# Performance work log

Measured on AMD Instinct MI355X. Metric: run time of the kernel, lower is better.

Reference implementation:

```python
import jax, jax.numpy as jnp
import numpy as np

HIDDEN = 128
STATE = 64
ACTION = 16
D_IO = STATE + ACTION  # 80
BATCH = 4096
SEQ_LEN = 512


def setup_inputs() -> dict:
    key = jax.random.key(0)
    ks = jax.random.split(key, 7)
    s = 1.0 / np.sqrt(HIDDEN)
    return {
        "quantized_hn": jax.random.normal(ks[0], (BATCH, HIDDEN), jnp.float32),
        "W_ih": jax.random.uniform(ks[1], (4 * HIDDEN, D_IO), jnp.float32, -s, s),
        "W_hh": jax.random.uniform(ks[2], (4 * HIDDEN, HIDDEN), jnp.float32, -s, s),
        "b_ih": jax.random.uniform(ks[3], (4 * HIDDEN,), jnp.float32, -s, s),
        "b_hh": jax.random.uniform(ks[4], (4 * HIDDEN,), jnp.float32, -s, s),
        "W_fc": jax.random.uniform(ks[5], (D_IO, HIDDEN), jnp.float32, -s, s),
        "b_fc": jax.random.uniform(ks[6], (D_IO,), jnp.float32, -s, s),
        "seq_len": SEQ_LEN,
    }


def reference(quantized_hn, W_ih, W_hh, b_ih, b_hh, W_fc, b_fc, seq_len):
    B, H = quantized_hn.shape
    D = W_fc.shape[0]

    def step(carry, _):
        h, c, x = carry  # h,c: (B,H); x: (B,D)
        # PyTorch LSTM gate order: i, f, g, o
        gates = x @ W_ih.T + b_ih + h @ W_hh.T + b_hh  # (B, 4H)
        i, f, g, o = jnp.split(gates, 4, axis=-1)
        c_new = jax.nn.sigmoid(f) * c + jax.nn.sigmoid(i) * jnp.tanh(g)
        h_new = jax.nn.sigmoid(o) * jnp.tanh(c_new)
        y = h_new @ W_fc.T + b_fc  # (B, D) -> fed back as next input
        return (h_new, c_new, y), y

    h0 = quantized_hn
    c0 = jnp.zeros((B, H), quantized_hn.dtype)
    x0 = jnp.zeros((B, D), quantized_hn.dtype)
    _, ys = jax.lax.scan(step, (h0, c0, x0), None, length=seq_len)
    return jnp.transpose(ys, (1, 0, 2))  # (B, seq_len, D)
```

## Files before the change

### kernel.cpp

```cpp
#include <hip/hip_runtime.h>

typedef __bf16 bf16_t;
typedef __bf16 bf16x4 __attribute__((ext_vector_type(4)));
typedef __bf16 bf16x8 __attribute__((ext_vector_type(8)));
typedef float  f32x4  __attribute__((ext_vector_type(4)));

#define HID    128
#define DIO    80
#define G4     512
#define TSTEP  512
#define BB     16
#define NBATCH 4096
#define NBLK   (NBATCH / BB)
#define HSTR   136

#define NL2E  -1.4426950408889634f
#define P2L2E  2.8853900817779268f

__device__ bf16_t g_weff_frags[128 * 512];
__device__ bf16_t g_whh_frags[128 * 512];
__device__ bf16_t g_wfc_frags[20 * 512];
__device__ float  g_weff[G4 * HID];
__device__ float  g_beff[G4];
__device__ float  g_b1[G4];

__global__ void k_weff(const float* __restrict__ W_ih, const float* __restrict__ W_hh,
                       const float* __restrict__ b_ih, const float* __restrict__ b_hh,
                       const float* __restrict__ W_fc, const float* __restrict__ b_fc) {
  int gid = blockIdx.x * blockDim.x + threadIdx.x;
  int g = gid >> 7, k = gid & 127;
  float sc = ((g >> 7) == 2) ? P2L2E : NL2E;
  float acc = W_hh[g * HID + k];
#pragma unroll 8
  for (int d = 0; d < DIO; ++d)
    acc = fmaf(W_ih[g * DIO + d], W_fc[d * HID + k], acc);
  g_weff[g * HID + k] = acc * sc;
  if (k == 0) {
    float bb = b_ih[g] + b_hh[g];
    g_b1[g] = bb * sc;
    float be = bb;
    for (int d = 0; d < DIO; ++d) be = fmaf(W_ih[g * DIO + d], b_fc[d], be);
    g_beff[g] = be * sc;
  }
}

__global__ void k_frag(const float* __restrict__ W_hh, const float* __restrict__ W_fc) {
  int tile = blockIdx.x;
  int lane = threadIdx.x;
  int c = lane & 15, q = lane >> 4;
  if (tile < 128) {
    int gtile = tile >> 2, kt = tile & 3;
    int n = gtile * 16 + c;
#pragma unroll
    for (int j = 0; j < 8; ++j)
      g_weff_frags[tile * 512 + lane * 8 + j] = (bf16_t)g_weff[n * HID + kt * 32 + q * 8 + j];
  } else if (tile < 256) {
    int t2 = tile - 128;
    int gtile = t2 >> 2, kt = t2 & 3;
    int n = gtile * 16 + c;
    float sc = ((n >> 7) == 2) ? P2L2E : NL2E;
#pragma unroll
    for (int j = 0; j < 8; ++j)
      g_whh_frags[t2 * 512 + lane * 8 + j] = (bf16_t)(W_hh[n * HID + kt * 32 + q * 8 + j] * sc);
  } else {
    int t2 = tile - 256;
    int yt = t2 >> 2, kt = t2 & 3;
    int n = yt * 16 + c;
#pragma unroll
    for (int j = 0; j < 8; ++j)
      g_wfc_frags[t2 * 512 + lane * 8 + j] = (bf16_t)W_fc[n * HID + kt * 32 + q * 8 + j];
  }
}

__device__ __forceinline__ float fexp2(float x) { return __builtin_amdgcn_exp2f(x); }
__device__ __forceinline__ float frcp(float x)  { return __builtin_amdgcn_rcpf(x); }

#define MFMA16(A, B, C) __builtin_amdgcn_mfma_f32_16x16x32_bf16((A), (B), (C), 0, 0, 0)

#define TAILR(ACC, CST, HV, R)                                                         \
  do {                                                                                 \
    float Eg = fexp2(ACC[2][R]);                                             \
    float ag = 1.0f + Eg;                                                              \
    float Ei = fexp2(ACC[0][R]);                                             \
    float ai = 1.0f + Ei;                                                              \
    float Ef = fexp2(ACC[1][R]);                                             \
    float af = 1.0f + Ef;                                                              \
    float P1 = ai * ag;                                                                \
    float Rr = frcp(P1 * af);                                                          \
    float tg = __builtin_fmaf(Eg, P2L2E, -P2L2E);                       \
    float m2 = tg * af;                                                                \
    float u  = __builtin_fmaf(P1, CST[R], m2);                                         \
    float cn = u * Rr;                             \
    CST[R] = cn;                                                                       \
    float cc = fminf(cn, 80.0f);                              \
    float Ec = fexp2(cc);                                                    \
    float Eo = fexp2(ACC[3][R]);                                             \
    float R2 = frcp((1.0f + Eo) * (1.0f + Ec));                                        \
    HV[R] = (bf16_t)((Ec - 1.0f) * R2);                            \
  } while (0)

#define GKT_FIRST(K, SRC)                                                              \
  acc[0] = MFMA16(Wg[0][K], SRC, bias[0]); acc[1] = MFMA16(Wg[1][K], SRC, bias[1]);    \
  acc[2] = MFMA16(Wg[2][K], SRC, bias[2]); acc[3] = MFMA16(Wg[3][K], SRC, bias[3]);
#define GKT(K, SRC)                                                                    \
  acc[0] = MFMA16(Wg[0][K], SRC, acc[0]); acc[1] = MFMA16(Wg[1][K], SRC, acc[1]);      \
  acc[2] = MFMA16(Wg[2][K], SRC, acc[2]); acc[3] = MFMA16(Wg[3][K], SRC, acc[3]);

#define YEMIT(PRV)                                                                     \
  { f32x4 ya = MFMA16(Wy[0], PRV[0], ybias); ya = MFMA16(Wy[1], PRV[1], ya);           \
    ya = MFMA16(Wy[2], PRV[2], ya); ya = MFMA16(Wy[3], PRV[3], ya);                    \
    *(f32x4*)outp = ya; outp += DIO; }

__device__ __forceinline__ void poll_ge(volatile unsigned* vf, int base, unsigned need) {
  for (;;) {
    unsigned a = vf[base + 0], b = vf[base + 1], x = vf[base + 2], d = vf[base + 3];
    unsigned m0 = a < b ? a : b, m1 = x < d ? x : d;
    if ((m0 < m1 ? m0 : m1) >= need) break;
  }
  __builtin_amdgcn_sched_barrier(0);
}

__global__ __launch_bounds__(512, 2) void k_lstm(const float* __restrict__ h0,
                                                 const float* __restrict__ b_fc,
                                                 float* __restrict__ out) {
  __shared__ __align__(16) bf16_t hbuf[2][BB * HSTR];
  __shared__ unsigned hflags[8];
  volatile unsigned* vf = hflags;
  const int tid = threadIdx.x;
  const int lane = tid & 63;
  const int w = tid >> 6;
  const int c = lane & 15, q = lane >> 4;
  const int b0 = blockIdx.x * BB;
  const bool isHigh = (w >= 4);

  for (int i = tid; i < BB * HID; i += 512) {
    int r = i >> 7, k = i & 127;
    hbuf[0][r * HSTR + k] = (bf16_t)h0[(long)(b0 + r) * HID + k];
  }
  if (lane == 0) hflags[w] = 1;

  bf16x8 Wy[4];
  f32x4  ybias;
  if (w < 5) {
#pragma unroll
    for (int kt = 0; kt < 4; ++kt)
      Wy[kt] = *(const bf16x8*)&g_wfc_frags[(w * 4 + kt) * 512 + lane * 8];
#pragma unroll
    for (int r = 0; r < 4; ++r) ybias[r] = b_fc[w * 16 + q * 4 + r];
  }

  bf16x8 Wg[4][4];
  f32x4  bias[4];
  auto load_wg = [&](const bf16_t* frags, const float* bsrc) {
#pragma unroll
    for (int G = 0; G < 4; ++G) {
      int gtile = G * 8 + w;
#pragma unroll
      for (int r = 0; r < 4; ++r) bias[G][r] = bsrc[gtile * 16 + q * 4 + r];
#pragma unroll
      for (int kt = 0; kt < 4; ++kt)
        Wg[G][kt] = *(const bf16x8*)&frags[(gtile * 4 + kt) * 512 + lane * 8];
    }
  };

  f32x4 cst = (f32x4){0, 0, 0, 0};
  bf16x8 hfA[4], hfB[4];

  load_wg(g_whh_frags, g_b1);
  __syncthreads();

  float* outp = out + (long)(b0 + c) * TSTEP * DIO + w * 16 + q * 4;

#pragma unroll
  for (int kt = 0; kt < 4; ++kt)
    hfA[kt] = *(const bf16x8*)&hbuf[0][c * HSTR + kt * 32 + q * 8];
  {
    f32x4 acc[4];
    GKT_FIRST(0, hfA[0]); GKT(1, hfA[1]); GKT(2, hfA[2]); GKT(3, hfA[3]);
    bf16x4 hv;
    TAILR(acc, cst, hv, 0); TAILR(acc, cst, hv, 1);
    TAILR(acc, cst, hv, 2); TAILR(acc, cst, hv, 3);
    *(bf16x4*)&hbuf[1][c * HSTR + w * 16 + q * 4] = hv;
    asm volatile("s_waitcnt lgkmcnt(0)" ::: "memory");
    if (lane == 0) vf[w] = 2;
  }
  load_wg(g_weff_frags, g_beff);

#define ITER(RD, PR, T, EMIT)                                                          \
  do {                                                                                 \
    const int rb = ((T)-1) & 1, wb = (T)&1;                                            \
    f32x4 acc[4];                                                                      \
    if (!isHigh) {                                                                     \
      poll_ge(vf, 0, (unsigned)(T));                                                   \
      RD[0] = *(const bf16x8*)&hbuf[rb][c * HSTR + 0 * 32 + q * 8];                    \
      RD[1] = *(const bf16x8*)&hbuf[rb][c * HSTR + 1 * 32 + q * 8];                    \
      GKT_FIRST(0, RD[0]); GKT(1, RD[1]);                                              \
      poll_ge(vf, 4, (unsigned)(T));                                                   \
      RD[2] = *(const bf16x8*)&hbuf[rb][c * HSTR + 2 * 32 + q * 8];                    \
      RD[3] = *(const bf16x8*)&hbuf[rb][c * HSTR + 3 * 32 + q * 8];                    \
      if ((EMIT) && w < 5) YEMIT(PR);                                                  \
      GKT(2, RD[2]); GKT(3, RD[3]);                                                    \
    } else {                                                                           \
      poll_ge(vf, 4, (unsigned)(T));                                                   \
      RD[2] = *(const bf16x8*)&hbuf[rb][c * HSTR + 2 * 32 + q * 8];                    \
      RD[3] = *(const bf16x8*)&hbuf[rb][c * HSTR + 3 * 32 + q * 8];                    \
      GKT_FIRST(2, RD[2]); GKT(3, RD[3]);                                              \
      poll_ge(vf, 0, (unsigned)(T));                                                   \
      RD[0] = *(const bf16x8*)&hbuf[rb][c * HSTR + 0 * 32 + q * 8];                    \
      RD[1] = *(const bf16x8*)&hbuf[rb][c * HSTR + 1 * 32 + q * 8];                    \
      if ((EMIT) && w < 5) YEMIT(PR);                                                  \
      GKT(0, RD[0]); GKT(1, RD[1]);                                                    \
    }                                                                                  \
    bf16x4 hv;                                                                         \
    TAILR(acc, cst, hv, 0); TAILR(acc, cst, hv, 1);                                    \
    TAILR(acc, cst, hv, 2); TAILR(acc, cst, hv, 3);                                    \
    *(bf16x4*)&hbuf[wb][c * HSTR + w * 16 + q * 4] = hv;                     \
    asm volatile("s_waitcnt lgkmcnt(0)" ::: "memory");                                 \
    if (lane == 0) vf[w] = (unsigned)((T) + 1);                                        \
  } while (0)

  ITER(hfB, hfA, 2, false);
  for (int p = 0; p < 255; ++p) {
    ITER(hfA, hfB, 3 + 2 * p, true);
    ITER(hfB, hfA, 4 + 2 * p, true);
  }

  if (w < 5) {
    YEMIT(hfB);
    poll_ge(vf, 0, 513u);
    poll_ge(vf, 4, 513u);
#pragma unroll
    for (int kt = 0; kt < 4; ++kt)
      hfA[kt] = *(const bf16x8*)&hbuf[0][c * HSTR + kt * 32 + q * 8];
    f32x4 ya = MFMA16(Wy[0], hfA[0], ybias);
    ya = MFMA16(Wy[1], hfA[1], ya);
    ya = MFMA16(Wy[2], hfA[2], ya);
    ya = MFMA16(Wy[3], hfA[3], ya);
    *(f32x4*)outp = ya;
  }
#undef ITER
}

extern "C" void kernel_launch(void* const* d_in, const int* in_sizes, int n_in,
                              void* d_out, int out_size, void* d_ws, size_t ws_size,
                              hipStream_t stream) {
  const float* h0   = (const float*)d_in[0];
  const float* W_ih = (const float*)d_in[1];
  const float* W_hh = (const float*)d_in[2];
  const float* b_ih = (const float*)d_in[3];
  const float* b_hh = (const float*)d_in[4];
  const float* W_fc = (const float*)d_in[5];
  const float* b_fc = (const float*)d_in[6];
  float* out = (float*)d_out;

  k_weff<<<256, 256, 0, stream>>>(W_ih, W_hh, b_ih, b_hh, W_fc, b_fc);
  k_frag<<<276, 64, 0, stream>>>(W_hh, W_fc);
  k_lstm<<<NBLK, 512, 0, stream>>>(h0, b_fc, out);
}
```

Measured before the change: 1.026 ms.

## Use per-k-tile paired 16-bit flags with staggered waits, sleep polling and priority

Replaces the 8 per-wave 32-bit flags with 16-bit flags packed in pairs, so each 32-bit read covers the two waves producing one 32-column k-tile. Each wave waits for and consumes k-tiles one at a time, starting with a rotated tile order (w>>1), so it can begin its MFMAs as soon as any producer pair has finished instead of waiting for groups of four waves. Spin loops now call s_sleep, and waves 0-3 get raised priority. The rotation is meant to cut synchronization stalls in the recurrent dependency. The costs are four polls per step instead of two, sleep latency on wakeups, and code size from the four-way unrolled RUN variants.

```diff
diff --git a/kernel.cpp b/kernel.cpp
--- a/kernel.cpp
+++ b/kernel.cpp
@@ -111,33 +111,33 @@
     ya = MFMA16(Wy[2], PRV[2], ya); ya = MFMA16(Wy[3], PRV[3], ya);                    \
     *(f32x4*)outp = ya; outp += DIO; }
 
-__device__ __forceinline__ void poll_ge(volatile unsigned* vf, int base, unsigned need) {
-  for (;;) {
-    unsigned a = vf[base + 0], b = vf[base + 1], x = vf[base + 2], d = vf[base + 3];
-    unsigned m0 = a < b ? a : b, m1 = x < d ? x : d;
-    if ((m0 < m1 ? m0 : m1) >= need) break;
-  }
-  __builtin_amdgcn_sched_barrier(0);
-}
+#define POLLP(K, NEED)                                                                 \
+  do {                                                                                 \
+    unsigned _pw = vfp[K];                                                             \
+    if ((_pw & 0xFFFFu) < (unsigned)(NEED) || (_pw >> 16) < (unsigned)(NEED)) {        \
+      do { __builtin_amdgcn_s_sleep(1); _pw = vfp[K]; }                                \
+      while ((_pw & 0xFFFFu) < (unsigned)(NEED) || (_pw >> 16) < (unsigned)(NEED));    \
+    }                                                                                  \
+    __builtin_amdgcn_sched_barrier(0);                                                 \
+  } while (0)
 
 __global__ __launch_bounds__(512, 2) void k_lstm(const float* __restrict__ h0,
                                                  const float* __restrict__ b_fc,
                                                  float* __restrict__ out) {
   __shared__ __align__(16) bf16_t hbuf[2][BB * HSTR];
-  __shared__ unsigned hflags[8];
-  volatile unsigned* vf = hflags;
+  __shared__ __align__(4) unsigned short hfl[8];
+  volatile unsigned* vfp = (volatile unsigned*)hfl;
   const int tid = threadIdx.x;
   const int lane = tid & 63;
   const int w = tid >> 6;
   const int c = lane & 15, q = lane >> 4;
   const int b0 = blockIdx.x * BB;
-  const bool isHigh = (w >= 4);
 
   for (int i = tid; i < BB * HID; i += 512) {
     int r = i >> 7, k = i & 127;
     hbuf[0][r * HSTR + k] = (bf16_t)h0[(long)(b0 + r) * HID + k];
   }
-  if (lane == 0) hflags[w] = 1;
+  if (tid < 8) hfl[tid] = 1;
 
   bf16x8 Wy[4];
   f32x4  ybias;
@@ -168,6 +168,8 @@
 
   load_wg(g_whh_frags, g_b1);
   __syncthreads();
+
+  if (w < 4) __builtin_amdgcn_s_setprio(1);
 
   float* outp = out + (long)(b0 + c) * TSTEP * DIO + w * 16 + q * 4;
 
@@ -182,63 +184,60 @@
     TAILR(acc, cst, hv, 2); TAILR(acc, cst, hv, 3);
     *(bf16x4*)&hbuf[1][c * HSTR + w * 16 + q * 4] = hv;
     asm volatile("s_waitcnt lgkmcnt(0)" ::: "memory");
-    if (lane == 0) vf[w] = 2;
+    if (lane == 0) ((volatile unsigned short*)hfl)[w] = 2;
   }
   load_wg(g_weff_frags, g_beff);
 
-#define ITER(RD, PR, T, EMIT)                                                          \
+#define ITER_K(RD, PR, T, EMIT, KA, KB, KC, KD)                                        \
   do {                                                                                 \
     const int rb = ((T)-1) & 1, wb = (T)&1;                                            \
     f32x4 acc[4];                                                                      \
-    if (!isHigh) {                                                                     \
-      poll_ge(vf, 0, (unsigned)(T));                                                   \
-      RD[0] = *(const bf16x8*)&hbuf[rb][c * HSTR + 0 * 32 + q * 8];                    \
-      RD[1] = *(const bf16x8*)&hbuf[rb][c * HSTR + 1 * 32 + q * 8];                    \
-      GKT_FIRST(0, RD[0]); GKT(1, RD[1]);                                              \
-      poll_ge(vf, 4, (unsigned)(T));                                                   \
-      RD[2] = *(const bf16x8*)&hbuf[rb][c * HSTR + 2 * 32 + q * 8];                    \
-      RD[3] = *(const bf16x8*)&hbuf[rb][c * HSTR + 3 * 32 + q * 8];                    \
-      if ((EMIT) && w < 5) YEMIT(PR);                                                  \
-      GKT(2, RD[2]); GKT(3, RD[3]);                                                    \
-    } else {                                                                           \
-      poll_ge(vf, 4, (unsigned)(T));                                                   \
-      RD[2] = *(const bf16x8*)&hbuf[rb][c * HSTR + 2 * 32 + q * 8];                    \
-      RD[3] = *(const bf16x8*)&hbuf[rb][c * HSTR + 3 * 32 + q * 8];                    \
-      GKT_FIRST(2, RD[2]); GKT(3, RD[3]);                                              \
-      poll_ge(vf, 0, (unsigned)(T));                                                   \
-      RD[0] = *(const bf16x8*)&hbuf[rb][c * HSTR + 0 * 32 + q * 8];                    \
-      RD[1] = *(const bf16x8*)&hbuf[rb][c * HSTR + 1 * 32 + q * 8];                    \
-      if ((EMIT) && w < 5) YEMIT(PR);                                                  \
-      GKT(0, RD[0]); GKT(1, RD[1]);                                                    \
-    }                                                                                  \
+    POLLP(KA, (T));                                                                    \
+    RD[KA] = *(const bf16x8*)&hbuf[rb][c * HSTR + (KA) * 32 + q * 8];                  \
+    GKT_FIRST(KA, RD[KA]);                                                             \
+    POLLP(KB, (T));                                                                    \
+    RD[KB] = *(const bf16x8*)&hbuf[rb][c * HSTR + (KB) * 32 + q * 8];                  \
+    GKT(KB, RD[KB]);                                                                   \
+    POLLP(KC, (T));                                                                    \
+    RD[KC] = *(const bf16x8*)&hbuf[rb][c * HSTR + (KC) * 32 + q * 8];                  \
+    GKT(KC, RD[KC]);                                                                   \
+    if ((EMIT) && w < 5) YEMIT(PR);                                                    \
+    POLLP(KD, (T));                                                                    \
+    RD[KD] = *(const bf16x8*)&hbuf[rb][c * HSTR + (KD) * 32 + q * 8];                  \
+    GKT(KD, RD[KD]);                                                                   \
     bf16x4 hv;                                                                         \
     TAILR(acc, cst, hv, 0); TAILR(acc, cst, hv, 1);                                    \
     TAILR(acc, cst, hv, 2); TAILR(acc, cst, hv, 3);                                    \
     *(bf16x4*)&hbuf[wb][c * HSTR + w * 16 + q * 4] = hv;                     \
     asm volatile("s_waitcnt lgkmcnt(0)" ::: "memory");                                 \
-    if (lane == 0) vf[w] = (unsigned)((T) + 1);                                        \
-  } while (0)
-
-  ITER(hfB, hfA, 2, false);
-  for (int p = 0; p < 255; ++p) {
-    ITER(hfA, hfB, 3 + 2 * p, true);
-    ITER(hfB, hfA, 4 + 2 * p, true);
-  }
+    if (lane == 0) ((volatile unsigned short*)hfl)[w] = (unsigned short)((T) + 1);     \
+  } while (0)
+
+#define RUN(KA, KB, KC, KD)                                                            \
+  do {                                                                                 \
+    ITER_K(hfB, hfA, 2, false, KA, KB, KC, KD);                                        \
+    for (int p = 0; p < 255; ++p) {                                                    \
+      ITER_K(hfA, hfB, 3 + 2 * p, true, KA, KB, KC, KD);                               \
+      ITER_K(hfB, hfA, 4 + 2 * p, true, KA, KB, KC, KD);                               \
+    }                                                                                  \
+  } while (0)
+
+  const int k0 = w >> 1;
+  if (k0 == 0)      RUN(0, 1, 2, 3);
+  else if (k0 == 1) RUN(1, 2, 3, 0);
+  else if (k0 == 2) RUN(2, 3, 0, 1);
+  else              RUN(3, 0, 1, 2);
 
   if (w < 5) {
     YEMIT(hfB);
-    poll_ge(vf, 0, 513u);
-    poll_ge(vf, 4, 513u);
+    POLLP(0, 513); POLLP(1, 513); POLLP(2, 513); POLLP(3, 513);
 #pragma unroll
     for (int kt = 0; kt < 4; ++kt)
       hfA[kt] = *(const bf16x8*)&hbuf[0][c * HSTR + kt * 32 + q * 8];
-    f32x4 ya = MFMA16(Wy[0], hfA[0], ybias);
-    ya = MFMA16(Wy[1], hfA[1], ya);
-    ya = MFMA16(Wy[2], hfA[2], ya);
-    ya = MFMA16(Wy[3], hfA[3], ya);
-    *(f32x4*)outp = ya;
-  }
-#undef ITER
+    YEMIT(hfA);
+  }
+#undef RUN
+#undef ITER_K
 }
 
 extern "C" void kernel_launch(void* const* d_in, const int* in_sizes, int n_in,
```

Result: no change. 1.023 ms (-0.3%).
